# Performance work log

Hardware: AMD Instinct MI355X
Metric: run time of the kernel (lower is better)

The kernel has to match this reference:

```python
import jax, jax.numpy as jnp
import numpy as np

H = 5  # hidden size (hardcoded in the torch module)


def setup_inputs() -> dict:
    key = jax.random.key(0)
    ks = jax.random.split(key, 9)
    N, T = 32768, 600
    s = 1.0 / np.sqrt(H)  # torch LSTM/Linear init scale (uniform bound), use as stddev
    return {
        "x": jax.random.normal(ks[0], (N, T), dtype=jnp.float32),
        "w_ih": jax.random.normal(ks[1], (4 * H, 1), dtype=jnp.float32) * s,
        "w_hh": jax.random.normal(ks[2], (4 * H, H), dtype=jnp.float32) * s,
        "b_ih": jax.random.normal(ks[3], (4 * H,), dtype=jnp.float32) * s,
        "b_hh": jax.random.normal(ks[4], (4 * H,), dtype=jnp.float32) * s,
        "fc_w": jax.random.normal(ks[5], (15, H), dtype=jnp.float32) * s,
        "fc_b": jax.random.normal(ks[6], (15,), dtype=jnp.float32) * s,
        "out_w": jax.random.normal(ks[7], (1, 15), dtype=jnp.float32) * (1.0 / np.sqrt(15)),
        "out_b": jax.random.normal(ks[8], (1,), dtype=jnp.float32) * (1.0 / np.sqrt(15)),
    }


def reference(x, w_ih, w_hh, b_ih, b_hh, fc_w, fc_b, out_w, out_b):
    # x: (N, T) -> unsqueeze to feature dim of 1 is implicit (input_size=1).
    N = x.shape[0]
    b = b_ih + b_hh  # (4H,)
    w_ih_vec = w_ih[:, 0]  # (4H,) since input_size == 1

    def step(carry, x_t):
        h, c = carry  # (N, H) each
        # gates: (N, 4H); PyTorch gate order: i, f, g, o
        gates = x_t[:, None] * w_ih_vec + h @ w_hh.T + b
        i = jax.nn.sigmoid(gates[:, 0 * H:1 * H])
        f = jax.nn.sigmoid(gates[:, 1 * H:2 * H])
        g = jnp.tanh(gates[:, 2 * H:3 * H])
        o = jax.nn.sigmoid(gates[:, 3 * H:4 * H])
        c = f * c + i * g
        h = o * jnp.tanh(c)
        return (h, c), None

    h0 = jnp.zeros((N, H), dtype=x.dtype)
    c0 = jnp.zeros((N, H), dtype=x.dtype)
    (h_T, _), _ = jax.lax.scan(step, (h0, c0), x.T)  # scan over time: xs (T, N)
    # Head: only the last timestep's hidden state is used.
    hid = h_T @ fc_w.T + fc_b          # (N, 15)
    out = hid @ out_w.T + out_b        # (N, 1)
    return jax.nn.sigmoid(out)
```

## Files before the change

### kernel.cpp

```cpp
#include <hip/hip_runtime.h>
#include <math.h>


#define LOG2E 1.44269504088896340736f

typedef float v2f __attribute__((ext_vector_type(2)));

constexpr int T_ = 600;
constexpr int SEQ_PER_BLOCK = 32;
constexpr int TTILE = 64;
constexpr int LDS_STRIDE = 68;

__device__ __forceinline__ float fast_rcp(float v)  { return __builtin_amdgcn_rcpf(v); }
__device__ __forceinline__ float fast_exp2(float v) { return __builtin_amdgcn_exp2f(v); }

__device__ __forceinline__ float dpp_swap1(float v) {
    const int x = __float_as_int(v);
    return __int_as_float(__builtin_amdgcn_update_dpp(x, x, 0xB1, 0xF, 0xF, false));
}

__global__ __launch_bounds__(64, 1) void lstm_kernel(
    const float* __restrict__ x,
    const float* __restrict__ w_ih,
    const float* __restrict__ w_hh,
    const float* __restrict__ b_ih,
    const float* __restrict__ b_hh,
    const float* __restrict__ fc_w,
    const float* __restrict__ fc_b,
    const float* __restrict__ out_w,
    const float* __restrict__ out_b,
    float* __restrict__ out)
{
    __shared__ float xs[SEQ_PER_BLOCK * LDS_STRIDE];

    const int lane = threadIdx.x;
    const int s    = lane >> 1;
    const int half = lane & 1;
    const int seq  = blockIdx.x * SEQ_PER_BLOCK + s;

    const float slo = -LOG2E;
    const float shi = half ? -LOG2E : -2.0f * LOG2E;
    v2f wih2[5], bb2[5], whh2[5][5];
#pragma unroll
    for (int p = 0; p < 5; ++p) {
        const int rlo = half * 5 + p;
        const int rhi = 10 + half * 5 + p;
        wih2[p] = (v2f){ w_ih[rlo] * slo, w_ih[rhi] * shi };
        bb2[p]  = (v2f){ (b_ih[rlo] + b_hh[rlo]) * slo,
                         (b_ih[rhi] + b_hh[rhi]) * shi };
#pragma unroll
        for (int k = 0; k < 5; ++k)
            whh2[p][k] = (v2f){ w_hh[rlo * 5 + k] * slo, w_hh[rhi * 5 + k] * shi };
    }
    const float Ahi = half ? 1.0f : (-4.0f * LOG2E);
    const float Bhi = half ? 0.0f : ( 2.0f * LOG2E);

    float h[5] = {0.f, 0.f, 0.f, 0.f, 0.f};
    float c[5] = {0.f, 0.f, 0.f, 0.f, 0.f};

    const float* xblk = x + (size_t)(blockIdx.x * SEQ_PER_BLOCK) * T_;

    auto step = [&](float xt) {
        const v2f x2 = (v2f){ xt, xt };
        v2f g2[5];
#pragma unroll
        for (int p = 0; p < 5; ++p) g2[p] = x2 * wih2[p] + bb2[p];
#pragma unroll
        for (int k = 0; k < 5; ++k) {
            const v2f h2 = (v2f){ h[k], h[k] };
#pragma unroll
            for (int p = 0; p < 5; ++p) g2[p] += h2 * whh2[p][k];
        }
        float actl[5], acth[5];
#pragma unroll
        for (int p = 0; p < 5; ++p) {
            const float dl = 1.0f + fast_exp2(g2[p].x);
            const float dh = 1.0f + fast_exp2(g2[p].y);
            const float rp = fast_rcp(dl * dh);
            actl[p] = rp * dh;
            acth[p] = fmaf(rp * dl, Ahi, Bhi);
        }
        float sl[5], sh[5];
#pragma unroll
        for (int k = 0; k < 5; ++k) { sl[k] = dpp_swap1(actl[k]); sh[k] = dpp_swap1(acth[k]); }
        float d[5], ov[5];
#pragma unroll
        for (int k = 0; k < 5; ++k) {
            const float t0 = actl[k] * acth[k];
            const float t1 = sl[k] * sh[k];
            const float ig = half ? t1 : t0;
            const float fv = half ? actl[k] : sl[k];
            ov[k]          = half ? acth[k] : sh[k];
            c[k] = fmaf(fv, c[k], ig);
            d[k] = 1.0f + fast_exp2(c[k]);
        }
        {
            const float i01 = fast_rcp(d[0] * d[1]);
            const float i23 = fast_rcp(d[2] * d[3]);
            const float i4  = fast_rcp(d[4]);
            const float r0 = i01 * d[1], r1 = i01 * d[0];
            const float r2 = i23 * d[3], r3 = i23 * d[2];
            h[0] = ov[0] * fmaf(r0, 2.0f, -1.0f);
            h[1] = ov[1] * fmaf(r1, 2.0f, -1.0f);
            h[2] = ov[2] * fmaf(r2, 2.0f, -1.0f);
            h[3] = ov[3] * fmaf(r3, 2.0f, -1.0f);
            h[4] = ov[4] * fmaf(i4, 2.0f, -1.0f);
        }
    };

    const int rrow = lane >> 4;
    const int ccol = (lane & 15) << 2;

    for (int t0 = 0; t0 < T_; t0 += TTILE) {
        __syncthreads();
#pragma unroll
        for (int it = 0; it < 8; ++it) {
            const int r = it * 4 + rrow;
            if (t0 + ccol < T_) {
                const float4 v = *(const float4*)(xblk + (size_t)r * T_ + (t0 + ccol));
                *(float4*)&xs[r * LDS_STRIDE + ccol] = v;
            }
        }
        __syncthreads();

        const int steps = min(TTILE, T_ - t0);
        const float* xr = &xs[s * LDS_STRIDE];
        for (int tt = 0; tt < steps; tt += 4) {
            const float4 xv4 = *(const float4*)&xr[tt];
            step(xv4.x);
            step(xv4.y);
            step(xv4.z);
            step(xv4.w);
        }
    }

    if (half == 0) {
        float acc = out_b[0];
#pragma unroll
        for (int j = 0; j < 15; ++j) {
            float hid = fc_b[j];
#pragma unroll
            for (int k = 0; k < 5; ++k) hid = fmaf(h[k], fc_w[j * 5 + k], hid);
            acc = fmaf(hid, out_w[j], acc);
        }
        out[seq] = fast_rcp(1.0f + fast_exp2(-acc * LOG2E));
    }
}

extern "C" void kernel_launch(void* const* d_in, const int* in_sizes, int n_in,
                              void* d_out, int out_size, void* d_ws, size_t ws_size,
                              hipStream_t stream) {
    const float* x    = (const float*)d_in[0];
    const float* w_ih = (const float*)d_in[1];
    const float* w_hh = (const float*)d_in[2];
    const float* b_ih = (const float*)d_in[3];
    const float* b_hh = (const float*)d_in[4];
    const float* fc_w = (const float*)d_in[5];
    const float* fc_b = (const float*)d_in[6];
    const float* out_w = (const float*)d_in[7];
    const float* out_b = (const float*)d_in[8];
    float* out = (float*)d_out;

    const int N = in_sizes[0] / T_;
    const int grid = N / SEQ_PER_BLOCK;
    hipLaunchKernelGGL(lstm_kernel, dim3(grid), dim3(64), 0, stream,
                       x, w_ih, w_hh, b_ih, b_hh, fc_w, fc_b, out_w, out_b, out);
}
```

Before: 286.5 us.

## Split LSTM cell-state update across lane pair instead of duplicating it

Previously both lanes of a pair computed all five cell-state and tanh(c) updates redundantly. Now each lane owns a subset (lane 0 units 0-2, lane 1 units 3-4), and DPP quad permutes exchange the products, forget gates and output gates. Broadcasts then reassemble the full hidden vector in both lanes. This cuts the transcendental and FMA work in the serial critical path, at the cost of more DPP moves and extra cross-lane dependency latency per step.

```diff
diff --git a/kernel.cpp b/kernel.cpp
--- a/kernel.cpp
+++ b/kernel.cpp
@@ -14,9 +14,10 @@
 __device__ __forceinline__ float fast_rcp(float v)  { return __builtin_amdgcn_rcpf(v); }
 __device__ __forceinline__ float fast_exp2(float v) { return __builtin_amdgcn_exp2f(v); }
 
-__device__ __forceinline__ float dpp_swap1(float v) {
+template <int CTRL>
+__device__ __forceinline__ float dpp_q(float v) {
     const int x = __float_as_int(v);
-    return __int_as_float(__builtin_amdgcn_update_dpp(x, x, 0xB1, 0xF, 0xF, false));
+    return __int_as_float(__builtin_amdgcn_update_dpp(x, x, CTRL, 0xF, 0xF, false));
 }
 
 __global__ __launch_bounds__(64, 1) void lstm_kernel(
@@ -55,8 +56,8 @@
     const float Ahi = half ? 1.0f : (-4.0f * LOG2E);
     const float Bhi = half ? 0.0f : ( 2.0f * LOG2E);
 
-    float h[5] = {0.f, 0.f, 0.f, 0.f, 0.f};
-    float c[5] = {0.f, 0.f, 0.f, 0.f, 0.f};
+    float H[5]  = {0.f, 0.f, 0.f, 0.f, 0.f};
+    float cS[3] = {0.f, 0.f, 0.f};
 
     const float* xblk = x + (size_t)(blockIdx.x * SEQ_PER_BLOCK) * T_;
 
@@ -67,7 +68,7 @@
         for (int p = 0; p < 5; ++p) g2[p] = x2 * wih2[p] + bb2[p];
 #pragma unroll
         for (int k = 0; k < 5; ++k) {
-            const v2f h2 = (v2f){ h[k], h[k] };
+            const v2f h2 = (v2f){ H[k], H[k] };
 #pragma unroll
             for (int p = 0; p < 5; ++p) g2[p] += h2 * whh2[p][k];
         }
@@ -80,50 +81,62 @@
             actl[p] = rp * dh;
             acth[p] = fmaf(rp * dl, Ahi, Bhi);
         }
-        float sl[5], sh[5];
+        float P[5];
 #pragma unroll
-        for (int k = 0; k < 5; ++k) { sl[k] = dpp_swap1(actl[k]); sh[k] = dpp_swap1(acth[k]); }
-        float d[5], ov[5];
-#pragma unroll
-        for (int k = 0; k < 5; ++k) {
-            const float t0 = actl[k] * acth[k];
-            const float t1 = sl[k] * sh[k];
-            const float ig = half ? t1 : t0;
-            const float fv = half ? actl[k] : sl[k];
-            ov[k]          = half ? acth[k] : sh[k];
-            c[k] = fmaf(fv, c[k], ig);
-            d[k] = 1.0f + fast_exp2(c[k]);
-        }
-        {
-            const float i01 = fast_rcp(d[0] * d[1]);
-            const float i23 = fast_rcp(d[2] * d[3]);
-            const float i4  = fast_rcp(d[4]);
-            const float r0 = i01 * d[1], r1 = i01 * d[0];
-            const float r2 = i23 * d[3], r3 = i23 * d[2];
-            h[0] = ov[0] * fmaf(r0, 2.0f, -1.0f);
-            h[1] = ov[1] * fmaf(r1, 2.0f, -1.0f);
-            h[2] = ov[2] * fmaf(r2, 2.0f, -1.0f);
-            h[3] = ov[3] * fmaf(r3, 2.0f, -1.0f);
-            h[4] = ov[4] * fmaf(i4, 2.0f, -1.0f);
-        }
+        for (int k = 0; k < 5; ++k) P[k] = actl[k] * acth[k];
+        const float P3b = dpp_q<0xA0>(P[3]);
+        const float P4b = dpp_q<0xA0>(P[4]);
+        const float P2b = dpp_q<0xA0>(P[2]);
+        const float f0b = dpp_q<0xF5>(actl[0]);
+        const float f1b = dpp_q<0xF5>(actl[1]);
+        const float f2b = dpp_q<0xF5>(actl[2]);
+        const float Pp0 = half ? P3b : P[0];
+        const float Pp1 = half ? P4b : P[1];
+        const float F0  = half ? actl[3] : f0b;
+        const float F1  = half ? actl[4] : f1b;
+        cS[0] = fmaf(F0,  cS[0], Pp0);
+        cS[1] = fmaf(F1,  cS[1], Pp1);
+        cS[2] = fmaf(f2b, cS[2], P2b);
+        const float d0 = 1.0f + fast_exp2(cS[0]);
+        const float d1 = 1.0f + fast_exp2(cS[1]);
+        const float d2 = 1.0f + fast_exp2(cS[2]);
+        const float q  = fast_rcp(d0 * d1);
+        const float r0 = q * d1, r1 = q * d0;
+        const float r2 = fast_rcp(d2);
+        const float t0 = fmaf(r0, 2.0f, -1.0f);
+        const float t1 = fmaf(r1, 2.0f, -1.0f);
+        const float t2 = fmaf(r2, 2.0f, -1.0f);
+        const float o0b = dpp_q<0xF5>(acth[0]);
+        const float o1b = dpp_q<0xF5>(acth[1]);
+        const float o2b = dpp_q<0xF5>(acth[2]);
+        const float O0 = half ? acth[3] : o0b;
+        const float O1 = half ? acth[4] : o1b;
+        const float hp0 = O0  * t0;
+        const float hp1 = O1  * t1;
+        const float hp2 = o2b * t2;
+        H[0] = dpp_q<0xA0>(hp0);
+        H[1] = dpp_q<0xA0>(hp1);
+        H[2] = dpp_q<0xA0>(hp2);
+        H[3] = dpp_q<0xF5>(hp0);
+        H[4] = dpp_q<0xF5>(hp1);
     };
 
     const int rrow = lane >> 4;
     const int ccol = (lane & 15) << 2;
 
-    for (int t0 = 0; t0 < T_; t0 += TTILE) {
+    for (int t0i = 0; t0i < T_; t0i += TTILE) {
         __syncthreads();
 #pragma unroll
         for (int it = 0; it < 8; ++it) {
             const int r = it * 4 + rrow;
-            if (t0 + ccol < T_) {
-                const float4 v = *(const float4*)(xblk + (size_t)r * T_ + (t0 + ccol));
+            if (t0i + ccol < T_) {
+                const float4 v = *(const float4*)(xblk + (size_t)r * T_ + (t0i + ccol));
                 *(float4*)&xs[r * LDS_STRIDE + ccol] = v;
             }
         }
         __syncthreads();
 
-        const int steps = min(TTILE, T_ - t0);
+        const int steps = min(TTILE, T_ - t0i);
         const float* xr = &xs[s * LDS_STRIDE];
         for (int tt = 0; tt < steps; tt += 4) {
             const float4 xv4 = *(const float4*)&xr[tt];
@@ -140,7 +153,7 @@
         for (int j = 0; j < 15; ++j) {
             float hid = fc_b[j];
 #pragma unroll
-            for (int k = 0; k < 5; ++k) hid = fmaf(h[k], fc_w[j * 5 + k], hid);
+            for (int k = 0; k < 5; ++k) hid = fmaf(H[k], fc_w[j * 5 + k], hid);
             acc = fmaf(hid, out_w[j], acc);
         }
         out[seq] = fast_rcp(1.0f + fast_exp2(-acc * LOG2E));
```

Result: faster. 271.8 us (-5.1%).
